# Optimization experiments

Hardware: AMD Instinct MI355X
Metric: run time of the kernel (lower is better)

The kernel has to match this reference:

```python
import jax, jax.numpy as jnp
import numpy as np

NUM_HEADS = 16  # CLIP ViT-L num_attention_heads


def setup_inputs() -> dict:
    key = jax.random.key(0)
    ks = jax.random.split(key, 11)
    B, T, E = 16, 577, 1024
    d = {
        "hidden_states": jax.random.normal(ks[0], (B, T, E), jnp.float32),
        # token 'size' from prior merging steps; sizes are >= 1 in practice
        "size": jax.random.uniform(ks[1], (B, T), jnp.float32) + 1.0,
        "wq": jax.random.normal(ks[2], (E, E), jnp.float32) * (E ** -0.5),
        "bq": jax.random.normal(ks[3], (E,), jnp.float32) * 0.02,
        "wk": jax.random.normal(ks[4], (E, E), jnp.float32) * (E ** -0.5),
        "bk": jax.random.normal(ks[5], (E,), jnp.float32) * 0.02,
        "wv": jax.random.normal(ks[6], (E, E), jnp.float32) * (E ** -0.5),
        "bv": jax.random.normal(ks[7], (E,), jnp.float32) * 0.02,
        "wo": jax.random.normal(ks[8], (E, E), jnp.float32) * (E ** -0.5),
        "bo": jax.random.normal(ks[9], (E,), jnp.float32) * 0.02,
    }
    return d


def reference(hidden_states, size, wq, bq, wk, bk, wv, bv, wo, bo):
    B, T, E = hidden_states.shape
    H = NUM_HEADS
    D = E // H
    scale = D ** -0.5

    # torch nn.Linear: y = x @ W.T + b
    q = (hidden_states @ wq.T + bq) * scale
    k = hidden_states @ wk.T + bk
    v = hidden_states @ wv.T + bv

    def split_heads(x):  # [B,T,E] -> [B,H,T,D]
        return x.reshape(B, T, H, D).transpose(0, 2, 1, 3)

    qh, kh, vh = split_heads(q), split_heads(k), split_heads(v)

    # raw logits (before size bias), [B,H,T,T]
    attn_logits = jnp.einsum("bhtd,bhsd->bhts", qh, kh)

    # att_score: mean over the flattened bsz*num_heads dim, on raw logits
    att_score = attn_logits.mean(axis=(0, 1))  # [T,T]

    # additive log-size bias over keys
    attn_logits = attn_logits + jnp.log(size)[:, None, None, :]

    probs = jax.nn.softmax(attn_logits, axis=-1)  # dropout p=0 / eval
    out = jnp.einsum("bhts,bhsd->bhtd", probs, vh)
    out = out.transpose(0, 2, 1, 3).reshape(B, T, E)
    attn_output = out @ wo.T + bo

    # mean over heads of key states: [B,T,D]
    mean_keys = kh.mean(axis=1)

    return attn_output, mean_keys, att_score
```

## Files before the change

kernel.cpp:

```cpp
#include <hip/hip_runtime.h>
#include <hip/hip_bf16.h>
#include <math.h>

typedef __attribute__((ext_vector_type(8))) short s16x8;
typedef __attribute__((ext_vector_type(4))) short s16x4;
typedef __attribute__((ext_vector_type(4))) float f32x4;
typedef __attribute__((ext_vector_type(8))) __bf16 bf16x8;

#define MFMA16(a, b, c) __builtin_amdgcn_mfma_f32_16x16x32_bf16( \
    __builtin_bit_cast(bf16x8, (a)), __builtin_bit_cast(bf16x8, (b)), (c), 0, 0, 0)

__device__ __forceinline__ short f2b(float f) {
    __bf16 h = (__bf16)f;
    return __builtin_bit_cast(short, h);
}
__device__ __forceinline__ float b2f(short b) {
    union { unsigned u; float f; } x;
    x.u = ((unsigned)(unsigned short)b) << 16;
    return x.f;
}

__device__ __forceinline__ void gload16(const void* g, void* l) {
    __builtin_amdgcn_global_load_lds(
        (const __attribute__((address_space(1))) unsigned int*)g,
        (__attribute__((address_space(3))) unsigned int*)l, 16, 0, 0);
}

__global__ void k_f32_to_bf16(const float* __restrict__ in, short* __restrict__ out, long n) {
    long i = ((long)blockIdx.x * blockDim.x + threadIdx.x) * 4;
    long stride = (long)gridDim.x * blockDim.x * 4;
    for (; i < n; i += stride) {
        float4 v = *(const float4*)(in + i);
        s16x4 o = { f2b(v.x), f2b(v.y), f2b(v.z), f2b(v.w) };
        *(s16x4*)(out + i) = o;
    }
}

__global__ void k_wconv4(const float* __restrict__ w0, const float* __restrict__ w1,
                         const float* __restrict__ w2, const float* __restrict__ w3,
                         short* __restrict__ out, long n) {
    int wsel = blockIdx.y;
    const float* src = (wsel == 0) ? w0 : (wsel == 1) ? w1 : (wsel == 2) ? w2 : w3;
    short* dst = out + (long)wsel * n;
    long i = ((long)blockIdx.x * blockDim.x + threadIdx.x) * 4;
    if (i >= n) return;
    float4 v = *(const float4*)(src + i);
    s16x4 o = { f2b(v.x), f2b(v.y), f2b(v.z), f2b(v.w) };
    *(s16x4*)(dst + i) = o;
}

__global__ void k_sizepad(const float* __restrict__ size, float* __restrict__ out,
                          int B, int T, int SP) {
    int i = blockIdx.x * blockDim.x + threadIdx.x;
    if (i >= B * SP) return;
    int b = i / SP, s = i % SP;
    out[i] = (s < T) ? size[b * T + s] : 0.f;
}

struct StagePtrs {
    const char* ga[4];
    const char* gb[4];
    int ldo[4];
};
__device__ __forceinline__ StagePtrs make_stage(
    const short* __restrict__ A, const short* __restrict__ Bw,
    int M, int N, int K, int row0, int col0, int tid) {
    StagePtrs sp;
    int lane = tid & 63, wave = tid >> 6;
    #pragma unroll
    for (int i = 0; i < 4; ++i) {
        int cw = i * 256 + wave * 64;
        int c = cw + lane;
        int r = c >> 3;
        int cby = ((c & 7) * 16) ^ ((r & 7) << 4);
        int ra = row0 + r; ra = ra < M ? ra : M - 1;
        int rb = col0 + r; rb = rb < N ? rb : N - 1;
        sp.ga[i] = (const char*)(A + (long)ra * K) + cby;
        sp.gb[i] = (const char*)(Bw + (long)rb * K) + cby;
        sp.ldo[i] = cw * 8;
    }
    return sp;
}

template<bool ROUTE>
__global__ __launch_bounds__(256) void k_gemm4(
    const short* __restrict__ A, const short* __restrict__ Bw,
    const float* __restrict__ bb0, const float* __restrict__ bb1, const float* __restrict__ bb2,
    short* __restrict__ o0, short* __restrict__ o1, short* __restrict__ o2,
    float* __restrict__ Cf, int M, int N, int K, int Ntiles, float alpha0) {

    __shared__ short As[128 * 64];
    __shared__ short Bs[128 * 64];

    int nwg = gridDim.x, orig = blockIdx.x;
    int qq = nwg >> 3, rr = nwg & 7;
    int xcd = orig & 7, pos = orig >> 3;
    int wg = (xcd < rr ? xcd * (qq + 1) : rr * (qq + 1) + (xcd - rr) * qq) + pos;
    int bx = wg % Ntiles, by = wg / Ntiles;
    int row0 = by * 128, col0 = bx * 128;

    int tid = threadIdx.x;
    int lane = tid & 63, wave = tid >> 6;
    int wr = wave >> 1, wc = wave & 1;
    int lr = lane & 15, lg = lane >> 4;

    StagePtrs sp = make_stage(A, Bw, M, N, K, row0, col0, tid);

    f32x4 acc[4][4];
    #pragma unroll
    for (int i = 0; i < 4; i++)
        #pragma unroll
        for (int j = 0; j < 4; j++)
            #pragma unroll
            for (int q = 0; q < 4; q++) acc[i][j][q] = 0.f;

    int nt = K >> 6;
    for (int t = 0; t < nt; ++t) {
        __syncthreads();
        #pragma unroll
        for (int i = 0; i < 4; ++i) {
            gload16(sp.ga[i], &As[sp.ldo[i]]);
            gload16(sp.gb[i], &Bs[sp.ldo[i]]);
            sp.ga[i] += 128; sp.gb[i] += 128;
        }
        __syncthreads();
        #pragma unroll
        for (int ks = 0; ks < 2; ++ks) {
            s16x8 af[4], bfr[4];
            #pragma unroll
            for (int i = 0; i < 4; ++i) {
                int r = wr * 64 + i * 16 + lr;
                af[i] = *(const s16x8*)((const char*)As + r * 128 +
                        (((ks << 6) + (lg << 4)) ^ ((r & 7) << 4)));
            }
            #pragma unroll
            for (int j = 0; j < 4; ++j) {
                int r = wc * 64 + j * 16 + lr;
                bfr[j] = *(const s16x8*)((const char*)Bs + r * 128 +
                         (((ks << 6) + (lg << 4)) ^ ((r & 7) << 4)));
            }
            #pragma unroll
            for (int i = 0; i < 4; ++i)
                #pragma unroll
                for (int j = 0; j < 4; ++j)
                    acc[i][j] = MFMA16(af[i], bfr[j], acc[i][j]);
        }
    }

    #pragma unroll
    for (int i = 0; i < 4; i++) {
        int grow0 = row0 + wr * 64 + i * 16 + lg * 4;
        #pragma unroll
        for (int j = 0; j < 4; j++) {
            int gc = col0 + wc * 64 + j * 16 + lr;
            if (gc >= N) continue;
            if (ROUTE) {
                int which = gc >> 10, lc = gc & 1023;
                float bias = (which == 0 ? bb0 : which == 1 ? bb1 : bb2)[lc];
                float alpha = (which == 0) ? alpha0 : 1.0f;
                short* op = (which == 0 ? o0 : which == 1 ? o1 : o2);
                #pragma unroll
                for (int q = 0; q < 4; ++q) {
                    int r2 = grow0 + q;
                    if (r2 < M) op[(long)r2 * 1024 + lc] = f2b((acc[i][j][q] + bias) * alpha);
                }
            } else {
                float bias = bb0[gc];
                #pragma unroll
                for (int q = 0; q < 4; ++q) {
                    int r2 = grow0 + q;
                    if (r2 < M) Cf[(long)r2 * N + gc] = acc[i][j][q] + bias;
                }
            }
        }
    }
}

__global__ __launch_bounds__(256) void k_att(
    const short* __restrict__ q, const short* __restrict__ k,
    float* __restrict__ attp, int T, int E) {
    __shared__ short As[128 * 64];
    __shared__ short Bs[128 * 64];
    int z = blockIdx.z;
    const short* Ab = q + (long)z * T * E;
    const short* Bb = k + (long)z * T * E;
    float* Cf = attp + (long)z * T * T;
    int row0 = blockIdx.y * 128, col0 = blockIdx.x * 128;

    int tid = threadIdx.x;
    int lane = tid & 63, wave = tid >> 6;
    int wr = wave >> 1, wc = wave & 1;
    int lr = lane & 15, lg = lane >> 4;

    StagePtrs sp = make_stage(Ab, Bb, T, T, E, row0, col0, tid);

    f32x4 acc[4][4];
    #pragma unroll
    for (int i = 0; i < 4; i++)
        #pragma unroll
        for (int j = 0; j < 4; j++)
            #pragma unroll
            for (int q2 = 0; q2 < 4; q2++) acc[i][j][q2] = 0.f;

    int nt = E >> 6;
    for (int t = 0; t < nt; ++t) {
        __syncthreads();
        #pragma unroll
        for (int i = 0; i < 4; ++i) {
            gload16(sp.ga[i], &As[sp.ldo[i]]);
            gload16(sp.gb[i], &Bs[sp.ldo[i]]);
            sp.ga[i] += 128; sp.gb[i] += 128;
        }
        __syncthreads();
        #pragma unroll
        for (int ks = 0; ks < 2; ++ks) {
            s16x8 af[4], bfr[4];
            #pragma unroll
            for (int i = 0; i < 4; ++i) {
                int r = wr * 64 + i * 16 + lr;
                af[i] = *(const s16x8*)((const char*)As + r * 128 +
                        (((ks << 6) + (lg << 4)) ^ ((r & 7) << 4)));
            }
            #pragma unroll
            for (int j = 0; j < 4; ++j) {
                int r = wc * 64 + j * 16 + lr;
                bfr[j] = *(const s16x8*)((const char*)Bs + r * 128 +
                         (((ks << 6) + (lg << 4)) ^ ((r & 7) << 4)));
            }
            #pragma unroll
            for (int i = 0; i < 4; ++i)
                #pragma unroll
                for (int j = 0; j < 4; ++j)
                    acc[i][j] = MFMA16(af[i], bfr[j], acc[i][j]);
        }
    }
    #pragma unroll
    for (int i = 0; i < 4; i++) {
        int rbase = row0 + wr * 64 + i * 16 + lg * 4;
        #pragma unroll
        for (int j = 0; j < 4; j++) {
            int c = col0 + wc * 64 + j * 16 + lr;
            if (c >= T) continue;
            #pragma unroll
            for (int q2 = 0; q2 < 4; q2++) {
                int r = rbase + q2;
                if (r >= T) continue;
                Cf[(long)r * T + c] = acc[i][j][q2];
            }
        }
    }
}

__global__ void k_mean_keys8(const short* __restrict__ Kb, float* __restrict__ out, int BT) {
    int i = blockIdx.x * blockDim.x + threadIdx.x;
    if (i >= BT * 8) return;
    int bt = i >> 3, d0 = (i & 7) * 8;
    const short* p = Kb + (long)bt * 1024 + d0;
    float s[8] = {0.f, 0.f, 0.f, 0.f, 0.f, 0.f, 0.f, 0.f};
    #pragma unroll
    for (int h = 0; h < 16; ++h) {
        s16x8 v = *(const s16x8*)(p + h * 64);
        #pragma unroll
        for (int j = 0; j < 8; ++j) s[j] += b2f(v[j]);
    }
    float4 o0 = {s[0] * 0.0625f, s[1] * 0.0625f, s[2] * 0.0625f, s[3] * 0.0625f};
    float4 o1 = {s[4] * 0.0625f, s[5] * 0.0625f, s[6] * 0.0625f, s[7] * 0.0625f};
    *(float4*)(out + (long)bt * 64 + d0) = o0;
    *(float4*)(out + (long)bt * 64 + d0 + 4) = o1;
}

__global__ void k_att_reduce(const float* __restrict__ part, float* __restrict__ out,
                             int n, int nb, long stride) {
    int i = blockIdx.x * blockDim.x + threadIdx.x;
    if (i >= n) return;
    float s = 0.f;
    for (int b = 0; b < nb; ++b) s += part[(long)b * stride + i];
    out[i] = s * 0.002707606174062286f;
}

__global__ __launch_bounds__(256) void k_vtrans(const short* __restrict__ v, short* __restrict__ vt,
                                                const float* __restrict__ szp,
                                                int B, int T, int H, int TP, int SP) {
    int b = blockIdx.z, h = blockIdx.y, t0 = blockIdx.x * 64;
    __shared__ short Vs[64][68];
    __shared__ float Szs[64];
    int tid = threadIdx.x;
    if (tid < 64) Szs[tid] = szp[b * SP + t0 + tid];
    for (int c = tid; c < 512; c += 256) {
        int r = c >> 3, m = c & 7;
        s16x8 val = {0,0,0,0,0,0,0,0};
        if (t0 + r < T) val = *(const s16x8*)(v + ((long)(b * T + t0 + r)) * (H * 64) + h * 64 + m * 8);
        *(s16x8*)&Vs[r][m * 8] = val;
    }
    __syncthreads();
    for (int c = tid; c < 512; c += 256) {
        int d = c >> 3, mw = c & 7;
        s16x8 o;
        #pragma unroll
        for (int j = 0; j < 8; j++) o[j] = f2b(b2f(Vs[mw * 8 + j][d]) * Szs[mw * 8 + j]);
        *(s16x8*)(vt + ((long)((b * H + h) * 64 + d)) * TP + t0 + mw * 8) = o;
    }
}

__global__ __launch_bounds__(256) void k_flash(
    const short* __restrict__ Q, const short* __restrict__ Kb, const short* __restrict__ VT,
    const float* __restrict__ szp, short* __restrict__ Ctx,
    int B, int T, int E, int H, int SP, int TP, int NTQ) {
    int nwg = gridDim.x;
    int cpx = nwg >> 3;
    int wg = (blockIdx.x & 7) * cpx + (blockIdx.x >> 3);
    int tq = wg % NTQ, h = (wg / NTQ) % H, b = wg / (NTQ * H);
    int t0 = tq * 128;

    __shared__ short Ks[64][68];
    __shared__ short Vt[80][68];
    __shared__ short Ps[4][32][68];
    int tid = threadIdx.x, wid = tid >> 6, lane = tid & 63;
    int lr = lane & 15, lg = lane >> 4;

    for (int c = tid; c < 15 * 68; c += 256) Vt[65 + c / 68][c % 68] = 0;

    s16x8 aqf[2][2];
    #pragma unroll
    for (int i = 0; i < 2; ++i) {
        int t = t0 + wid * 32 + i * 16 + lr; t = t < T ? t : T - 1;
        #pragma unroll
        for (int ks = 0; ks < 2; ++ks)
            aqf[i][ks] = *(const s16x8*)(Q + ((long)b * T + t) * E + h * 64 + ks * 32 + lg * 8);
    }

    const short* kb  = Kb + (long)b * T * E + h * 64;
    const short* vtb = VT + ((long)(b * H + h)) * 64 * TP;

    int c0 = tid, c1 = tid + 256;
    int r0 = c0 >> 3, m0 = c0 & 7, r1 = c1 >> 3, m1 = c1 & 7;
    s16x8 kreg0, kreg1, vreg0, vreg1;
    float szreg = 0.f;

    {
        int s = r0; s = s < T ? s : T - 1;
        kreg0 = *(const s16x8*)(kb + (long)s * E + m0 * 8);
        s = r1; s = s < T ? s : T - 1;
        kreg1 = *(const s16x8*)(kb + (long)s * E + m1 * 8);
        vreg0 = *(const s16x8*)(vtb + (long)r0 * TP + 0 + m0 * 8);
        vreg1 = *(const s16x8*)(vtb + (long)r1 * TP + 0 + m1 * 8);
        if (tid < 64) szreg = szp[b * SP + 0 + tid];
    }

    float mreg[2][4];
    f32x4 o[2][5];
    #pragma unroll
    for (int i = 0; i < 2; i++)
        #pragma unroll
        for (int q = 0; q < 4; q++) mreg[i][q] = -INFINITY;
    #pragma unroll
    for (int i = 0; i < 2; i++)
        #pragma unroll
        for (int jd = 0; jd < 5; jd++)
            #pragma unroll
            for (int q = 0; q < 4; q++) o[i][jd][q] = 0.f;

    for (int s0 = 0; s0 < T; s0 += 64) {
        *(s16x8*)&Ks[r0][m0 * 8] = kreg0;
        *(s16x8*)&Ks[r1][m1 * 8] = kreg1;
        *(s16x8*)&Vt[r0][m0 * 8] = vreg0;
        *(s16x8*)&Vt[r1][m1 * 8] = vreg1;
        if (tid < 64) Vt[64][tid] = f2b(szreg);
        __syncthreads();

        if (s0 + 64 < T) {
            int sn = s0 + 64;
            int s = sn + r0; s = s < T ? s : T - 1;
            kreg0 = *(const s16x8*)(kb + (long)s * E + m0 * 8);
            s = sn + r1; s = s < T ? s : T - 1;
            kreg1 = *(const s16x8*)(kb + (long)s * E + m1 * 8);
            vreg0 = *(const s16x8*)(vtb + (long)r0 * TP + sn + m0 * 8);
            vreg1 = *(const s16x8*)(vtb + (long)r1 * TP + sn + m1 * 8);
            if (tid < 64) szreg = szp[b * SP + sn + tid];
        }

        s16x8 kf[2][4];
        #pragma unroll
        for (int ks = 0; ks < 2; ++ks)
            #pragma unroll
            for (int j = 0; j < 4; ++j)
                kf[ks][j] = *(const s16x8*)&Ks[j * 16 + lr][ks * 32 + lg * 8];

        #pragma unroll
        for (int i = 0; i < 2; ++i) {
            f32x4 sf[4];
            #pragma unroll
            for (int j = 0; j < 4; j++)
                #pragma unroll
                for (int q = 0; q < 4; q++) sf[j][q] = 0.f;
            __builtin_amdgcn_s_setprio(1);
            #pragma unroll
            for (int ks = 0; ks < 2; ++ks)
                #pragma unroll
                for (int j = 0; j < 4; j++) sf[j] = MFMA16(aqf[i][ks], kf[ks][j], sf[j]);
            __builtin_amdgcn_s_setprio(0);

            float tmax[4];
            #pragma unroll
            for (int q = 0; q < 4; q++)
                tmax[q] = fmaxf(fmaxf(sf[0][q], sf[1][q]), fmaxf(sf[2][q], sf[3][q]));
            int ok = 1;
            #pragma unroll
            for (int q = 0; q < 4; q++) ok &= (tmax[q] <= mreg[i][q] + 11.0f) ? 1 : 0;
            if (!__all(ok)) {
                #pragma unroll
                for (int q = 0; q < 4; q++) {
                    #pragma unroll
                    for (int msk = 1; msk < 16; msk <<= 1)
                        tmax[q] = fmaxf(tmax[q], __shfl_xor(tmax[q], msk));
                    float mn = fmaxf(mreg[i][q], tmax[q]);
                    float al = exp2f(mreg[i][q] - mn);
                    mreg[i][q] = mn;
                    #pragma unroll
                    for (int jd = 0; jd < 5; jd++) o[i][jd][q] *= al;
                }
            }
            #pragma unroll
            for (int j = 0; j < 4; j++)
                #pragma unroll
                for (int q = 0; q < 4; q++)
                    Ps[wid][i * 16 + lg * 4 + q][j * 16 + lr] = f2b(exp2f(sf[j][q] - mreg[i][q]));

            __builtin_amdgcn_s_setprio(1);
            #pragma unroll
            for (int ks = 0; ks < 2; ++ks) {
                s16x8 ap = *(const s16x8*)&Ps[wid][i * 16 + lr][ks * 32 + lg * 8];
                #pragma unroll
                for (int jd = 0; jd < 5; jd++) {
                    s16x8 bv = *(const s16x8*)&Vt[jd * 16 + lr][ks * 32 + lg * 8];
                    o[i][jd] = MFMA16(ap, bv, o[i][jd]);
                }
            }
            __builtin_amdgcn_s_setprio(0);
        }
        __syncthreads();
    }

    short* cb = Ctx + ((long)b * T + t0) * E + h * 64;
    #pragma unroll
    for (int i = 0; i < 2; i++)
        #pragma unroll
        for (int q = 0; q < 4; q++) {
            float s = __shfl(o[i][4][q], lane & 48);
            int t = wid * 32 + i * 16 + lg * 4 + q;
            if (t0 + t >= T) continue;
            float inv = 1.f / s;
            #pragma unroll
            for (int jd = 0; jd < 4; jd++)
                cb[(long)t * E + jd * 16 + lr] = f2b(o[i][jd][q] * inv);
        }
}

extern "C" void kernel_launch(void* const* d_in, const int* in_sizes, int n_in,
                              void* d_out, int out_size, void* d_ws, size_t ws_size,
                              hipStream_t stream) {
    (void)in_sizes; (void)n_in; (void)out_size; (void)ws_size;
    const int B = 16, T = 577, E = 1024, H = 16;
    const int SP = 640, TP = 640;
    const float* hs   = (const float*)d_in[0];
    const float* size = (const float*)d_in[1];
    const float* wq   = (const float*)d_in[2];
    const float* bq   = (const float*)d_in[3];
    const float* wk   = (const float*)d_in[4];
    const float* bk   = (const float*)d_in[5];
    const float* wv   = (const float*)d_in[6];
    const float* bv   = (const float*)d_in[7];
    const float* wo   = (const float*)d_in[8];
    const float* bo   = (const float*)d_in[9];

    float* out_attn = (float*)d_out;
    float* out_mk   = out_attn + (long)B * T * E;
    float* out_as   = out_mk + (long)B * T * 64;

    long nBTE = (long)B * T * E;
    long nEE  = (long)E * E;
    char* ws = (char*)d_ws;
    short* hs_b  = (short*)ws; ws += nBTE * 2;
    short* wq_b  = (short*)ws; ws += nEE * 2;
    short* wk_b  = (short*)ws; ws += nEE * 2;
    short* wv_b  = (short*)ws; ws += nEE * 2;
    short* wo_b  = (short*)ws; ws += nEE * 2;
    short* q_b   = (short*)ws; ws += nBTE * 2;
    short* k_b   = (short*)ws; ws += nBTE * 2;
    short* v_b   = (short*)ws; ws += nBTE * 2;
    short* ctx_b = (short*)ws; ws += nBTE * 2;
    float* szpad = (float*)ws; ws += (long)B * SP * 4;
    float* att_p = (float*)ws; ws += (long)B * T * T * 4;
    short* vt = (short*)att_p;

    k_f32_to_bf16<<<2048, 256, 0, stream>>>(hs, hs_b, nBTE);
    {
        dim3 gw((nEE / 4 + 255) / 256, 4);
        k_wconv4<<<gw, 256, 0, stream>>>(wq, wk, wv, wo, wq_b, nEE);
    }
    k_sizepad<<<(B * SP + 255) / 256, 256, 0, stream>>>(size, szpad, B, T, SP);

    int M = B * T;
    {
        int Mtiles = (M + 127) / 128, Ntiles = 3072 / 128;
        k_gemm4<true><<<Mtiles * Ntiles, 256, 0, stream>>>(
            hs_b, wq_b, bq, bk, bv, q_b, k_b, v_b, nullptr, M, 3072, E, Ntiles,
            0.18033688011112042f);
    }

    dim3 g_att((T + 127) / 128, (T + 127) / 128, B);
    k_att<<<g_att, dim3(256), 0, stream>>>(q_b, k_b, att_p, T, E);
    k_att_reduce<<<((T * T) + 255) / 256, 256, 0, stream>>>(att_p, out_as, T * T, B, (long)T * T);

    dim3 g_vt((T + 63) / 64, H, B);
    k_vtrans<<<g_vt, dim3(256), 0, stream>>>(v_b, vt, szpad, B, T, H, TP, SP);

    k_mean_keys8<<<((B * T * 8) + 255) / 256, 256, 0, stream>>>(k_b, out_mk, B * T);

    const int NTQ = (T + 127) / 128;
    int nfl = NTQ * H * B;
    k_flash<<<nfl, dim3(256), 0, stream>>>(q_b, k_b, vt, szpad, ctx_b, B, T, E, H, SP, TP, NTQ);

    {
        int Mtiles = (M + 127) / 128, Ntiles = 1024 / 128;
        k_gemm4<false><<<Mtiles * Ntiles, 256, 0, stream>>>(
            ctx_b, wo_b, bo, nullptr, nullptr, nullptr, nullptr, nullptr,
            out_attn, M, 1024, E, Ntiles, 1.0f);
    }
}
```

Before: 292.2 us.

## Double-buffer GEMM K-loop with 32-wide K tiles and prefetch

Replaces the single-buffered 64-wide K staging in the projection and QK^T GEMMs with a shared double-buffered core that loads 32-wide K slices into alternating LDS buffers. The next tile's loads are issued before the MFMAs on the current tile, with a single barrier per iteration and raised wave priority around the MFMA block. The intent is to hide global-to-LDS latency behind compute and halve LDS per buffer. The cost is twice as many loop iterations and barriers, plus a new swizzle for the 64-byte row layout.

New measurement: 290.6 us. About the same (-0.5%).

```diff
diff --git a/kernel.cpp b/kernel.cpp
--- a/kernel.cpp
+++ b/kernel.cpp
@@ -57,29 +57,80 @@
     out[i] = (s < T) ? size[b * T + s] : 0.f;
 }
 
-struct StagePtrs {
-    const char* ga[4];
-    const char* gb[4];
-    int ldo[4];
-};
-__device__ __forceinline__ StagePtrs make_stage(
+__device__ __forceinline__ void core32(
     const short* __restrict__ A, const short* __restrict__ Bw,
-    int M, int N, int K, int row0, int col0, int tid) {
-    StagePtrs sp;
+    int M, int N, int K, int row0, int col0,
+    short* AS, short* BS,
+    f32x4 acc[4][4]) {
+    int tid = threadIdx.x;
     int lane = tid & 63, wave = tid >> 6;
-    #pragma unroll
-    for (int i = 0; i < 4; ++i) {
-        int cw = i * 256 + wave * 64;
-        int c = cw + lane;
-        int r = c >> 3;
-        int cby = ((c & 7) * 16) ^ ((r & 7) << 4);
+    int wr = wave >> 1, wc = wave & 1;
+    int lr = lane & 15, lg = lane >> 4;
+
+    const char* ga[2]; const char* gb[2]; int ldo[2];
+    #pragma unroll
+    for (int j = 0; j < 2; ++j) {
+        int ch = j * 256 + wave * 64 + lane;
+        int r = ch >> 2, slot = ch & 3;
+        int cby = (slot << 4) ^ (((r >> 1) & 3) << 4);
         int ra = row0 + r; ra = ra < M ? ra : M - 1;
         int rb = col0 + r; rb = rb < N ? rb : N - 1;
-        sp.ga[i] = (const char*)(A + (long)ra * K) + cby;
-        sp.gb[i] = (const char*)(Bw + (long)rb * K) + cby;
-        sp.ldo[i] = cw * 8;
-    }
-    return sp;
+        ga[j] = (const char*)(A + (long)ra * K) + cby;
+        gb[j] = (const char*)(Bw + (long)rb * K) + cby;
+        ldo[j] = ch * 8;
+    }
+    #pragma unroll
+    for (int i = 0; i < 4; i++)
+        #pragma unroll
+        for (int j = 0; j < 4; j++)
+            #pragma unroll
+            for (int q = 0; q < 4; q++) acc[i][j][q] = 0.f;
+
+    #pragma unroll
+    for (int j = 0; j < 2; ++j) {
+        gload16(ga[j], AS + ldo[j]);
+        gload16(gb[j], BS + ldo[j]);
+        ga[j] += 64; gb[j] += 64;
+    }
+
+    int nt = K >> 5;
+    for (int t = 0; t < nt; ++t) {
+        int cur = t & 1;
+        asm volatile("s_waitcnt vmcnt(0)" ::: "memory");
+        __builtin_amdgcn_s_barrier();
+        if (t + 1 < nt) {
+            short* Ad = AS + (cur ^ 1) * 4096;
+            short* Bd = BS + (cur ^ 1) * 4096;
+            #pragma unroll
+            for (int j = 0; j < 2; ++j) {
+                gload16(ga[j], Ad + ldo[j]);
+                gload16(gb[j], Bd + ldo[j]);
+                ga[j] += 64; gb[j] += 64;
+            }
+        }
+        const short* Ab2 = AS + cur * 4096;
+        const short* Bb2 = BS + cur * 4096;
+        s16x8 af[4], bfr[4];
+        #pragma unroll
+        for (int i = 0; i < 4; ++i) {
+            int r = wr * 64 + i * 16 + lr;
+            af[i] = *(const s16x8*)((const char*)Ab2 + r * 64 +
+                    ((lg << 4) ^ (((r >> 1) & 3) << 4)));
+        }
+        #pragma unroll
+        for (int j = 0; j < 4; ++j) {
+            int r = wc * 64 + j * 16 + lr;
+            bfr[j] = *(const s16x8*)((const char*)Bb2 + r * 64 +
+                     ((lg << 4) ^ (((r >> 1) & 3) << 4)));
+        }
+        __builtin_amdgcn_s_setprio(1);
+        #pragma unroll
+        for (int i = 0; i < 4; ++i)
+            #pragma unroll
+            for (int j = 0; j < 4; ++j)
+                acc[i][j] = MFMA16(af[i], bfr[j], acc[i][j]);
+        __builtin_amdgcn_s_setprio(0);
+    }
 }
 
 template<bool ROUTE>
@@ -89,8 +140,8 @@
     short* __restrict__ o0, short* __restrict__ o1, short* __restrict__ o2,
     float* __restrict__ Cf, int M, int N, int K, int Ntiles, float alpha0) {
 
-    __shared__ short As[128 * 64];
-    __shared__ short Bs[128 * 64];
+    __shared__ short AS[2][128 * 32];
+    __shared__ short BS[2][128 * 32];
 
     int nwg = gridDim.x, orig = blockIdx.x;
     int qq = nwg >> 3, rr = nwg & 7;
@@ -104,48 +155,8 @@
     int wr = wave >> 1, wc = wave & 1;
     int lr = lane & 15, lg = lane >> 4;
 
-    StagePtrs sp = make_stage(A, Bw, M, N, K, row0, col0, tid);
-
     f32x4 acc[4][4];
-    #pragma unroll
-    for (int i = 0; i < 4; i++)
-        #pragma unroll
-        for (int j = 0; j < 4; j++)
-            #pragma unroll
-            for (int q = 0; q < 4; q++) acc[i][j][q] = 0.f;
-
-    int nt = K >> 6;
-    for (int t = 0; t < nt; ++t) {
-        __syncthreads();
-        #pragma unroll
-        for (int i = 0; i < 4; ++i) {
-            gload16(sp.ga[i], &As[sp.ldo[i]]);
-            gload16(sp.gb[i], &Bs[sp.ldo[i]]);
-            sp.ga[i] += 128; sp.gb[i] += 128;
-        }
-        __syncthreads();
-        #pragma unroll
-        for (int ks = 0; ks < 2; ++ks) {
-            s16x8 af[4], bfr[4];
-            #pragma unroll
-            for (int i = 0; i < 4; ++i) {
-                int r = wr * 64 + i * 16 + lr;
-                af[i] = *(const s16x8*)((const char*)As + r * 128 +
-                        (((ks << 6) + (lg << 4)) ^ ((r & 7) << 4)));
-            }
-            #pragma unroll
-            for (int j = 0; j < 4; ++j) {
-                int r = wc * 64 + j * 16 + lr;
-                bfr[j] = *(const s16x8*)((const char*)Bs + r * 128 +
-                         (((ks << 6) + (lg << 4)) ^ ((r & 7) << 4)));
-            }
-            #pragma unroll
-            for (int i = 0; i < 4; ++i)
-                #pragma unroll
-                for (int j = 0; j < 4; ++j)
-                    acc[i][j] = MFMA16(af[i], bfr[j], acc[i][j]);
-        }
-    }
+    core32(A, Bw, M, N, K, row0, col0, &AS[0][0], &BS[0][0], acc);
 
     #pragma unroll
     for (int i = 0; i < 4; i++) {
@@ -179,8 +190,8 @@
 __global__ __launch_bounds__(256) void k_att(
     const short* __restrict__ q, const short* __restrict__ k,
     float* __restrict__ attp, int T, int E) {
-    __shared__ short As[128 * 64];
-    __shared__ short Bs[128 * 64];
+    __shared__ short AS[2][128 * 32];
+    __shared__ short BS[2][128 * 32];
     int z = blockIdx.z;
     const short* Ab = q + (long)z * T * E;
     const short* Bb = k + (long)z * T * E;
@@ -192,48 +203,9 @@
     int wr = wave >> 1, wc = wave & 1;
     int lr = lane & 15, lg = lane >> 4;
 
-    StagePtrs sp = make_stage(Ab, Bb, T, T, E, row0, col0, tid);
-
     f32x4 acc[4][4];
-    #pragma unroll
-    for (int i = 0; i < 4; i++)
-        #pragma unroll
-        for (int j = 0; j < 4; j++)
-            #pragma unroll
-            for (int q2 = 0; q2 < 4; q2++) acc[i][j][q2] = 0.f;
-
-    int nt = E >> 6;
-    for (int t = 0; t < nt; ++t) {
-        __syncthreads();
-        #pragma unroll
-        for (int i = 0; i < 4; ++i) {
-            gload16(sp.ga[i], &As[sp.ldo[i]]);
-            gload16(sp.gb[i], &Bs[sp.ldo[i]]);
-            sp.ga[i] += 128; sp.gb[i] += 128;
-        }
-        __syncthreads();
-        #pragma unroll
-        for (int ks = 0; ks < 2; ++ks) {
-            s16x8 af[4], bfr[4];
-            #pragma unroll
-            for (int i = 0; i < 4; ++i) {
-                int r = wr * 64 + i * 16 + lr;
-                af[i] = *(const s16x8*)((const char*)As + r * 128 +
-                        (((ks << 6) + (lg << 4)) ^ ((r & 7) << 4)));
-            }
-            #pragma unroll
-            for (int j = 0; j < 4; ++j) {
-                int r = wc * 64 + j * 16 + lr;
-                bfr[j] = *(const s16x8*)((const char*)Bs + r * 128 +
-                         (((ks << 6) + (lg << 4)) ^ ((r & 7) << 4)));
-            }
-            #pragma unroll
-            for (int i = 0; i < 4; ++i)
-                #pragma unroll
-                for (int j = 0; j < 4; ++j)
-                    acc[i][j] = MFMA16(af[i], bfr[j], acc[i][j]);
-        }
-    }
+    core32(Ab, Bb, T, T, E, row0, col0, &AS[0][0], &BS[0][0], acc);
+
     #pragma unroll
     for (int i = 0; i < 4; i++) {
         int rbase = row0 + wr * 64 + i * 16 + lg * 4;
```
